# Optimization experiments

Measured on AMD Instinct MI355X. Metric: run time of the kernel, lower is better.

The kernel has to match this reference:

```python
import jax, jax.numpy as jnp
import numpy as np

NEG_SLOPE = 0.2
STRONG_CONVEXITY = 0.5


def _scalar(x, Wq, Wl, bl, Wz, wz_out, wq_out, wl_out):
    # x: [B, D]; Wq/Wl: [L, H, D]; bl: [L, H]; Wz: [L-1, H, H]
    # Precompute all per-layer x-dependent terms in two batched einsums.
    qx = jnp.einsum('lhd,bd->lbh', Wq, x) ** 2          # [L, B, H]
    lx = jnp.einsum('lhd,bd->lbh', Wl, x) + bl[:, None, :]  # [L, B, H]
    z = jax.nn.leaky_relu(qx[0] + lx[0], negative_slope=NEG_SLOPE)

    def step(z, inputs):
        W, q, l = inputs
        z = jax.nn.leaky_relu(z @ W.T + q + l, negative_slope=NEG_SLOPE)
        return z, None

    z, _ = jax.lax.scan(step, z, (Wz, qx[1:], lx[1:]))
    # Final layer to scalar output (no bias on last wx_lin per torch code).
    out = z @ wz_out.T + (x @ wq_out.T) ** 2 + x @ wl_out.T  # [B, 1]
    return out


def setup_inputs() -> dict:
    key = jax.random.key(0)
    ks = jax.random.split(key, 8)
    B, D, H, L = 8192, 128, 512, 10
    f32 = jnp.float32
    x = jax.random.normal(ks[0], (B, D), f32)
    Wq = jax.random.normal(ks[1], (L, H, D), f32) * (1.0 / np.sqrt(D))
    Wl = jax.random.normal(ks[2], (L, H, D), f32) * (1.0 / np.sqrt(D))
    bl = jax.random.normal(ks[3], (L, H), f32) * 0.01
    # wz weights are kept non-negative in the original (clamp/exp init)
    Wz = jnp.abs(jax.random.normal(ks[4], (L - 1, H, H), f32)) * (1.0 / np.sqrt(H))
    wz_out = jnp.abs(jax.random.normal(ks[5], (1, H), f32)) * (1.0 / np.sqrt(H))
    wq_out = jax.random.normal(ks[6], (1, D), f32) * (1.0 / np.sqrt(D))
    wl_out = jax.random.normal(ks[7], (1, D), f32) * (1.0 / np.sqrt(D))
    return {"x": x, "Wq": Wq, "Wl": Wl, "bl": bl, "Wz": Wz,
            "wz_out": wz_out, "wq_out": wq_out, "wl_out": wl_out}


def reference(x, Wq, Wl, bl, Wz, wz_out, wq_out, wl_out):
    # forward = (1 - mu) * d(scalar)/dx + mu * x, with grad_outputs = ones
    def scalar_sum(xx):
        return jnp.sum(_scalar(xx, Wq, Wl, bl, Wz, wz_out, wq_out, wl_out))

    gx = jax.grad(scalar_sum)(x)  # per-sample gradient, [B, D]
    return (1.0 - STRONG_CONVEXITY) * gx + STRONG_CONVEXITY * x
```

## Files before the change

### kernel.cpp

```cpp
#include <hip/hip_runtime.h>


#define Bn 8192
#define Dn 128
#define Hn 512
#define Ln 10
#define NW (Ln * Hn)

constexpr float NS = 0.2f;

typedef __attribute__((ext_vector_type(8))) short short8;
typedef __attribute__((ext_vector_type(4))) float f32x4;

typedef const __attribute__((address_space(1))) void GV;
typedef __attribute__((address_space(3))) void LV;

__device__ __forceinline__ void gload16(const void* g, void* l) {
    __builtin_amdgcn_global_load_lds((GV*)g, (LV*)l, 16, 0, 0);
}

#define MFMA(acc, a, b) acc = __builtin_amdgcn_mfma_f32_16x16x32_bf16(a, b, acc, 0, 0, 0)

__device__ __forceinline__ unsigned short bf16_rne(float v) {
    unsigned u = __float_as_uint(v);
    u += 0x7FFFu + ((u >> 16) & 1u);
    return (unsigned short)(u >> 16);
}
__device__ __forceinline__ float bf2f(unsigned short h) {
    return __uint_as_float(((unsigned)h) << 16);
}
__device__ __forceinline__ void split2(float v, unsigned short& h, unsigned short& l) {
    h = bf16_rne(v);
    l = bf16_rne(v - bf2f(h));
}


__global__ __launch_bounds__(256) void split_flat(const float* __restrict__ in,
        unsigned short* __restrict__ hi, unsigned short* __restrict__ lo, int n4) {
    int i = blockIdx.x * 256 + threadIdx.x;
    if (i >= n4) return;
    float4 v = ((const float4*)in)[i];
    ushort4 h, l;
    split2(v.x, h.x, l.x);
    split2(v.y, h.y, l.y);
    split2(v.z, h.z, l.z);
    split2(v.w, h.w, l.w);
    ((ushort4*)hi)[i] = h;
    ((ushort4*)lo)[i] = l;
}

__global__ __launch_bounds__(256) void transpose_split(const float* __restrict__ in,
        unsigned short* __restrict__ hi, unsigned short* __restrict__ lo, int R, int C) {
    __shared__ float t[32][33];
    const size_t off = (size_t)blockIdx.z * R * C;
    const float* src = in + off;
    unsigned short* dh = hi + off;
    unsigned short* dl = lo + off;
    const int r0 = blockIdx.x * 32, c0 = blockIdx.y * 32;
    const int tr = threadIdx.x >> 5, tc = threadIdx.x & 31;
#pragma unroll
    for (int i = 0; i < 4; ++i)
        t[tr + 8 * i][tc] = src[(size_t)(r0 + tr + 8 * i) * C + c0 + tc];
    __syncthreads();
#pragma unroll
    for (int i = 0; i < 4; ++i) {
        float v = t[tc][tr + 8 * i];
        unsigned short h, l; split2(v, h, l);
        size_t o = (size_t)(c0 + tr + 8 * i) * R + r0 + tc;
        dh[o] = h; dl[o] = l;
    }
}


__global__ __launch_bounds__(256) void gemm_uall(
    const unsigned short* __restrict__ xh, const unsigned short* __restrict__ xl,
    const unsigned short* __restrict__ Wh, const unsigned short* __restrict__ Wv,
    float* __restrict__ u)
{
    __shared__ __align__(16) char smem[32768];
    unsigned short* Ah = (unsigned short*)smem;
    unsigned short* Al = (unsigned short*)(smem + 8192);
    unsigned short* Bh = (unsigned short*)(smem + 16384);
    unsigned short* Bl = (unsigned short*)(smem + 24576);

    const int tid = threadIdx.x;
    const int w = tid >> 6, lane = tid & 63;
    const int lq = lane >> 4, lc = lane & 15;
    const int wm = (w & 1) * 64, wn = (w >> 1) * 64;
    const int row0 = blockIdx.x * 128, col0 = blockIdx.y * 128;
    const int sr = lane >> 2, sk = (lane & 3) * 8;

    f32x4 acc[4][4];
#pragma unroll
    for (int i = 0; i < 4; ++i)
#pragma unroll
        for (int j = 0; j < 4; ++j)
#pragma unroll
            for (int r = 0; r < 4; ++r) acc[i][j][r] = 0.f;

    for (int k0 = 0; k0 < Dn; k0 += 32) {
        __syncthreads();
        for (int c = w; c < 8; c += 4) {
            size_t ga_ = (size_t)(row0 + c * 16 + sr) * Dn + k0 + sk;
            gload16(xh + ga_, Ah + c * 512);
            gload16(xl + ga_, Al + c * 512);
            size_t gb = (size_t)(col0 + c * 16 + sr) * Dn + k0 + sk;
            gload16(Wh + gb, Bh + c * 512);
            gload16(Wv + gb, Bl + c * 512);
        }
        __syncthreads();
        short8 ah[4], al[4];
#pragma unroll
        for (int mt = 0; mt < 4; ++mt) {
            int ao = (wm + mt * 16 + lc) * 32 + lq * 8;
            ah[mt] = *(const short8*)(Ah + ao);
            al[mt] = *(const short8*)(Al + ao);
        }
#pragma unroll
        for (int nt = 0; nt < 4; ++nt) {
            int bo = (wn + nt * 16 + lc) * 32 + lq * 8;
            short8 bh = *(const short8*)(Bh + bo);
            short8 bv = *(const short8*)(Bl + bo);
#pragma unroll
            for (int mt = 0; mt < 4; ++mt) {
                MFMA(acc[mt][nt], ah[mt], bh);
                MFMA(acc[mt][nt], ah[mt], bv);
                MFMA(acc[mt][nt], al[mt], bh);
            }
        }
    }

#pragma unroll
    for (int nt = 0; nt < 4; ++nt) {
        const int col = col0 + wn + nt * 16 + lc;
#pragma unroll
        for (int mt = 0; mt < 4; ++mt) {
            const int rowb = row0 + wm + mt * 16;
#pragma unroll
            for (int r = 0; r < 4; ++r)
                u[(size_t)(rowb + lq * 4 + r) * NW + col] = acc[mt][nt][r];
        }
    }
}


__global__ __launch_bounds__(256) void fwd_mfma(
    const unsigned short* __restrict__ xh, const unsigned short* __restrict__ xl,
    const unsigned short* __restrict__ zph, const unsigned short* __restrict__ zpl,
    const unsigned short* __restrict__ Wzh, const unsigned short* __restrict__ Wzl,
    const unsigned short* __restrict__ Wlh, const unsigned short* __restrict__ Wll,
    const float* __restrict__ bl,
    const float* __restrict__ u,
    unsigned short* __restrict__ zoh, unsigned short* __restrict__ zol,
    unsigned short* __restrict__ mask16, int hasZ)
{
    __shared__ __align__(16) char smem[24576];
    unsigned short* Ah = (unsigned short*)smem;
    unsigned short* Al = (unsigned short*)(smem + 8192);
    unsigned short* Bh = (unsigned short*)(smem + 16384);
    unsigned short* Bl = (unsigned short*)(smem + 20480);

    const int tid = threadIdx.x;
    const int w = tid >> 6, lane = tid & 63;
    const int lq = lane >> 4, lc = lane & 15;
    const int wm = (w & 1) * 64, wn = (w >> 1) * 32;
    const int row0 = blockIdx.x * 128, col0 = blockIdx.y * 64;
    const int sr = lane >> 2, sk = (lane & 3) * 8;

    f32x4 acc[4][2];
#pragma unroll
    for (int i = 0; i < 4; ++i)
#pragma unroll
        for (int j = 0; j < 2; ++j)
#pragma unroll
            for (int r = 0; r < 4; ++r) acc[i][j][r] = 0.f;

    if (hasZ) {
        for (int k0 = 0; k0 < Hn; k0 += 32) {
            __syncthreads();
            for (int c = w; c < 8; c += 4) {
                size_t go = (size_t)(row0 + c * 16 + sr) * Hn + k0 + sk;
                gload16(zph + go, Ah + c * 512);
                gload16(zpl + go, Al + c * 512);
            }
            {
                int c = w;
                size_t go = (size_t)(col0 + c * 16 + sr) * Hn + k0 + sk;
                gload16(Wzh + go, Bh + c * 512);
                gload16(Wzl + go, Bl + c * 512);
            }
            __syncthreads();
            short8 ah[4], al[4];
#pragma unroll
            for (int mt = 0; mt < 4; ++mt) {
                int ao = (wm + mt * 16 + lc) * 32 + lq * 8;
                ah[mt] = *(const short8*)(Ah + ao);
                al[mt] = *(const short8*)(Al + ao);
            }
#pragma unroll
            for (int nt = 0; nt < 2; ++nt) {
                int bo = (wn + nt * 16 + lc) * 32 + lq * 8;
                short8 bh = *(const short8*)(Bh + bo);
                short8 bv = *(const short8*)(Bl + bo);
#pragma unroll
                for (int mt = 0; mt < 4; ++mt) {
                    MFMA(acc[mt][nt], ah[mt], bh);
                    MFMA(acc[mt][nt], ah[mt], bv);
                    MFMA(acc[mt][nt], al[mt], bh);
                }
            }
        }
    }

    for (int k0 = 0; k0 < Dn; k0 += 32) {
        __syncthreads();
        for (int c = w; c < 8; c += 4) {
            size_t go = (size_t)(row0 + c * 16 + sr) * Dn + k0 + sk;
            gload16(xh + go, Ah + c * 512);
            gload16(xl + go, Al + c * 512);
        }
        {
            int c = w;
            size_t go = (size_t)(col0 + c * 16 + sr) * Dn + k0 + sk;
            gload16(Wlh + go, Bh + c * 512);
            gload16(Wll + go, Bl + c * 512);
        }
        __syncthreads();
        short8 ah[4], al[4];
#pragma unroll
        for (int mt = 0; mt < 4; ++mt) {
            int ao = (wm + mt * 16 + lc) * 32 + lq * 8;
            ah[mt] = *(const short8*)(Ah + ao);
            al[mt] = *(const short8*)(Al + ao);
        }
#pragma unroll
        for (int nt = 0; nt < 2; ++nt) {
            int bo = (wn + nt * 16 + lc) * 32 + lq * 8;
            short8 bh = *(const short8*)(Bh + bo);
            short8 bv = *(const short8*)(Bl + bo);
#pragma unroll
            for (int mt = 0; mt < 4; ++mt) {
                MFMA(acc[mt][nt], ah[mt], bh);
                MFMA(acc[mt][nt], ah[mt], bv);
                MFMA(acc[mt][nt], al[mt], bh);
            }
        }
    }

#pragma unroll
    for (int nt = 0; nt < 2; ++nt) {
        const int colb = col0 + wn + nt * 16;
        const int col = colb + lc;
        const float blv = bl[col];
#pragma unroll
        for (int mt = 0; mt < 4; ++mt) {
            const int rowb = row0 + wm + mt * 16;
#pragma unroll
            for (int r = 0; r < 4; ++r) {
                const int row = rowb + lq * 4 + r;
                float uq = u[(size_t)row * NW + col];
                float pre = acc[mt][nt][r] + uq * uq + blv;
                bool m = pre >= 0.f;
                unsigned long long bal = __ballot(m);
                if (lc == 0) {
                    mask16[(size_t)row * 32 + (colb >> 4)] =
                        (unsigned short)((bal >> (lq * 16)) & 0xFFFFull);
                }
                float zv = m ? pre : NS * pre;
                unsigned short h, l; split2(zv, h, l);
                size_t o = (size_t)row * Hn + col;
                zoh[o] = h; zol[o] = l;
            }
        }
    }
}


__global__ __launch_bounds__(256) void bwd_mfma(
    const unsigned short* __restrict__ gah, const unsigned short* __restrict__ gal,
    const unsigned short* __restrict__ WzTh, const unsigned short* __restrict__ WzTl,
    const unsigned short* __restrict__ maskprev,
    unsigned short* __restrict__ goh, unsigned short* __restrict__ gol,
    const float* __restrict__ u,
    const unsigned short* __restrict__ WqTh, const unsigned short* __restrict__ WqTl,
    const unsigned short* __restrict__ WlTh, const unsigned short* __restrict__ WlTl,
    float* __restrict__ gx, int addTo, int nWz)
{
    __shared__ __align__(16) char smem[49152];
    const int tid = threadIdx.x;
    const int w = tid >> 6, lane = tid & 63;
    const int lq = lane >> 4, lc = lane & 15;
    const int wm = (w & 1) * 64, wn = (w >> 1) * 32;
    const int row0 = blockIdx.x * 128;
    const int sr = lane >> 2, sk = (lane & 3) * 8;

    f32x4 acc[4][2];
#pragma unroll
    for (int i = 0; i < 4; ++i)
#pragma unroll
        for (int j = 0; j < 2; ++j)
#pragma unroll
            for (int r = 0; r < 4; ++r) acc[i][j][r] = 0.f;

    if ((int)blockIdx.y < nWz) {
        const int col0 = blockIdx.y * 64;
        unsigned short* Ah = (unsigned short*)smem;
        unsigned short* Al = (unsigned short*)(smem + 8192);
        unsigned short* Bh = (unsigned short*)(smem + 16384);
        unsigned short* Bl = (unsigned short*)(smem + 20480);

        for (int k0 = 0; k0 < Hn; k0 += 32) {
            __syncthreads();
            for (int c = w; c < 8; c += 4) {
                size_t go = (size_t)(row0 + c * 16 + sr) * Hn + k0 + sk;
                gload16(gah + go, Ah + c * 512);
                gload16(gal + go, Al + c * 512);
            }
            {
                int c = w;
                size_t go = (size_t)(col0 + c * 16 + sr) * Hn + k0 + sk;
                gload16(WzTh + go, Bh + c * 512);
                gload16(WzTl + go, Bl + c * 512);
            }
            __syncthreads();
            short8 ah[4], al[4];
#pragma unroll
            for (int mt = 0; mt < 4; ++mt) {
                int ao = (wm + mt * 16 + lc) * 32 + lq * 8;
                ah[mt] = *(const short8*)(Ah + ao);
                al[mt] = *(const short8*)(Al + ao);
            }
#pragma unroll
            for (int nt = 0; nt < 2; ++nt) {
                int bo = (wn + nt * 16 + lc) * 32 + lq * 8;
                short8 bh = *(const short8*)(Bh + bo);
                short8 bv = *(const short8*)(Bl + bo);
#pragma unroll
                for (int mt = 0; mt < 4; ++mt) {
                    MFMA(acc[mt][nt], ah[mt], bh);
                    MFMA(acc[mt][nt], ah[mt], bv);
                    MFMA(acc[mt][nt], al[mt], bh);
                }
            }
        }

#pragma unroll
        for (int nt = 0; nt < 2; ++nt) {
            const int colb = col0 + wn + nt * 16;
            const int col = colb + lc;
#pragma unroll
            for (int mt = 0; mt < 4; ++mt) {
                const int rowb = row0 + wm + mt * 16;
#pragma unroll
                for (int r = 0; r < 4; ++r) {
                    int row = rowb + lq * 4 + r;
                    unsigned short wbits = maskprev[(size_t)row * 32 + (colb >> 4)];
                    float f = ((wbits >> lc) & 1) ? 1.f : NS;
                    float v = acc[mt][nt][r] * f;
                    unsigned short h, l; split2(v, h, l);
                    size_t o = (size_t)row * Hn + col;
                    goh[o] = h; gol[o] = l;
                }
            }
        }
    } else {
        const int col0 = ((int)blockIdx.y - nWz) * 64;
        unsigned short* A1h = (unsigned short*)smem;
        unsigned short* A1l = (unsigned short*)(smem + 8192);
        unsigned short* A2h = (unsigned short*)(smem + 16384);
        unsigned short* A2l = (unsigned short*)(smem + 24576);
        unsigned short* Bqh = (unsigned short*)(smem + 32768);
        unsigned short* Bql = (unsigned short*)(smem + 36864);
        unsigned short* Blh = (unsigned short*)(smem + 40960);
        unsigned short* Bll = (unsigned short*)(smem + 45056);

        const int ar = tid >> 1;
        const int as = (tid & 1) * 16;

        for (int k0 = 0; k0 < Hn; k0 += 32) {
            __syncthreads();
            {
                int c = w;
                size_t go = (size_t)(col0 + c * 16 + sr) * Hn + k0 + sk;
                gload16(WqTh + go, Bqh + c * 512);
                gload16(WqTl + go, Bql + c * 512);
                gload16(WlTh + go, Blh + c * 512);
                gload16(WlTl + go, Bll + c * 512);
            }
            {
                size_t gb = (size_t)(row0 + ar) * Hn + k0 + as;
                const float* urow = u + (size_t)(row0 + ar) * NW + k0 + as;
                int lo_ = ar * 32 + as;
#pragma unroll
                for (int t4 = 0; t4 < 4; ++t4) {
                    float4 uv = *(const float4*)(urow + t4 * 4);
                    ushort4 h = *(const ushort4*)(gah + gb + t4 * 4);
                    ushort4 lw = *(const ushort4*)(gal + gb + t4 * 4);
                    *(ushort4*)(A2h + lo_ + t4 * 4) = h;
                    *(ushort4*)(A2l + lo_ + t4 * 4) = lw;
                    ushort4 oh, ol;
                    float g, a1;
                    g = bf2f(h.x) + bf2f(lw.x); a1 = 2.f * uv.x * g; split2(a1, oh.x, ol.x);
                    g = bf2f(h.y) + bf2f(lw.y); a1 = 2.f * uv.y * g; split2(a1, oh.y, ol.y);
                    g = bf2f(h.z) + bf2f(lw.z); a1 = 2.f * uv.z * g; split2(a1, oh.z, ol.z);
                    g = bf2f(h.w) + bf2f(lw.w); a1 = 2.f * uv.w * g; split2(a1, oh.w, ol.w);
                    *(ushort4*)(A1h + lo_ + t4 * 4) = oh;
                    *(ushort4*)(A1l + lo_ + t4 * 4) = ol;
                }
            }
            __syncthreads();
            short8 a1h[4], a1l[4], a2h[4], a2l[4];
#pragma unroll
            for (int mt = 0; mt < 4; ++mt) {
                int ao = (wm + mt * 16 + lc) * 32 + lq * 8;
                a1h[mt] = *(const short8*)(A1h + ao);
                a1l[mt] = *(const short8*)(A1l + ao);
                a2h[mt] = *(const short8*)(A2h + ao);
                a2l[mt] = *(const short8*)(A2l + ao);
            }
#pragma unroll
            for (int nt = 0; nt < 2; ++nt) {
                int bo = (wn + nt * 16 + lc) * 32 + lq * 8;
                short8 qh = *(const short8*)(Bqh + bo);
                short8 ql_ = *(const short8*)(Bql + bo);
                short8 lh = *(const short8*)(Blh + bo);
                short8 ll_ = *(const short8*)(Bll + bo);
#pragma unroll
                for (int mt = 0; mt < 4; ++mt) {
                    MFMA(acc[mt][nt], a1h[mt], qh);
                    MFMA(acc[mt][nt], a1h[mt], ql_);
                    MFMA(acc[mt][nt], a1l[mt], qh);
                    MFMA(acc[mt][nt], a2h[mt], lh);
                    MFMA(acc[mt][nt], a2h[mt], ll_);
                    MFMA(acc[mt][nt], a2l[mt], lh);
                }
            }
        }

#pragma unroll
        for (int nt = 0; nt < 2; ++nt) {
            const int col = col0 + wn + nt * 16 + lc;
#pragma unroll
            for (int mt = 0; mt < 4; ++mt) {
                const int rowb = row0 + wm + mt * 16;
#pragma unroll
                for (int r = 0; r < 4; ++r) {
                    size_t o = (size_t)(rowb + lq * 4 + r) * Dn + col;
                    float v = acc[mt][nt][r];
                    if (addTo) v += gx[o];
                    gx[o] = v;
                }
            }
        }
    }
}


__global__ __launch_bounds__(256) void ga_init(
    const float* __restrict__ wz_out, const unsigned short* __restrict__ mask9,
    unsigned short* __restrict__ gh, unsigned short* __restrict__ gl)
{
    int i = blockIdx.x * 256 + threadIdx.x;
    int e = i << 2;
    int b = e >> 9, h = e & 511;
    unsigned short wbits = mask9[(size_t)b * 32 + (h >> 4)];
    float4 wv = *(const float4*)(wz_out + h);
    int sh = h & 15;
    ushort4 oh, ol;
    float f;
    f = wv.x * (((wbits >> (sh + 0)) & 1) ? 1.f : NS); split2(f, oh.x, ol.x);
    f = wv.y * (((wbits >> (sh + 1)) & 1) ? 1.f : NS); split2(f, oh.y, ol.y);
    f = wv.z * (((wbits >> (sh + 2)) & 1) ? 1.f : NS); split2(f, oh.z, ol.z);
    f = wv.w * (((wbits >> (sh + 3)) & 1) ? 1.f : NS); split2(f, oh.w, ol.w);
    *(ushort4*)(gh + e) = oh;
    *(ushort4*)(gl + e) = ol;
}

__global__ __launch_bounds__(256) void rowdot_kernel(
    const float* __restrict__ x, const float* __restrict__ wq_out, float* __restrict__ s) {
    const int b = blockIdx.x * 4 + (threadIdx.x >> 6);
    const int lane = threadIdx.x & 63;
    float v = x[(size_t)b * Dn + lane] * wq_out[lane] +
              x[(size_t)b * Dn + 64 + lane] * wq_out[64 + lane];
#pragma unroll
    for (int off = 32; off > 0; off >>= 1) v += __shfl_down(v, off, 64);
    if (lane == 0) s[b] = v;
}

__global__ __launch_bounds__(256) void final_kernel(
    float* __restrict__ out, const float* __restrict__ x, const float* __restrict__ s,
    const float* __restrict__ wq_out, const float* __restrict__ wl_out) {
    const int i = blockIdx.x * 256 + threadIdx.x;
    const int base = i << 2;
    const int b = base >> 7;
    const int d = base & (Dn - 1);
    float4 g = *(const float4*)(out + base);
    float4 xv = *(const float4*)(x + base);
    float4 wq = *(const float4*)(wq_out + d);
    float4 wl = *(const float4*)(wl_out + d);
    const float sb = s[b];
    float4 o;
    o.x = 0.5f * g.x + sb * wq.x + 0.5f * wl.x + 0.5f * xv.x;
    o.y = 0.5f * g.y + sb * wq.y + 0.5f * wl.y + 0.5f * xv.y;
    o.z = 0.5f * g.z + sb * wq.z + 0.5f * wl.z + 0.5f * xv.z;
    o.w = 0.5f * g.w + sb * wq.w + 0.5f * wl.w + 0.5f * xv.w;
    *(float4*)(out + base) = o;
}


extern "C" void kernel_launch(void* const* d_in, const int* in_sizes, int n_in,
                              void* d_out, int out_size, void* d_ws, size_t ws_size,
                              hipStream_t stream) {
    (void)in_sizes; (void)n_in; (void)out_size; (void)ws_size;
    const float* x      = (const float*)d_in[0];
    const float* Wq     = (const float*)d_in[1];
    const float* Wl     = (const float*)d_in[2];
    const float* bl     = (const float*)d_in[3];
    const float* Wz     = (const float*)d_in[4];
    const float* wz_out = (const float*)d_in[5];
    const float* wq_out = (const float*)d_in[6];
    const float* wl_out = (const float*)d_in[7];
    float* out = (float*)d_out;

    char* p = (char*)d_ws;
    #define CARVE(name, bytes) unsigned short* name = (unsigned short*)p; p += (((size_t)(bytes)) + 255) & ~(size_t)255;
    CARVE(xh,  (size_t)Bn*Dn*2)  CARVE(xl,  (size_t)Bn*Dn*2)
    CARVE(Wqh, (size_t)Ln*Hn*Dn*2) CARVE(Wql, (size_t)Ln*Hn*Dn*2)
    CARVE(Wlh, (size_t)Ln*Hn*Dn*2) CARVE(Wll, (size_t)Ln*Hn*Dn*2)
    CARVE(WqTh,(size_t)Ln*Hn*Dn*2) CARVE(WqTl,(size_t)Ln*Hn*Dn*2)
    CARVE(WlTh,(size_t)Ln*Hn*Dn*2) CARVE(WlTl,(size_t)Ln*Hn*Dn*2)
    CARVE(Wzh, (size_t)(Ln-1)*Hn*Hn*2) CARVE(Wzl, (size_t)(Ln-1)*Hn*Hn*2)
    CARVE(WzTh,(size_t)(Ln-1)*Hn*Hn*2) CARVE(WzTl,(size_t)(Ln-1)*Hn*Hn*2)
    CARVE(zAh, (size_t)Bn*Hn*2) CARVE(zAl, (size_t)Bn*Hn*2)
    CARVE(zBh, (size_t)Bn*Hn*2) CARVE(zBl, (size_t)Bn*Hn*2)
    CARVE(mask16, (size_t)Ln*Bn*32*2)
    float* s = (float*)p; p += (size_t)Bn*4 + 256;
    float* uall = (float*)p; p += (size_t)Bn*NW*4;
    #undef CARVE

    split_flat<<<(Bn*Dn/4 + 255)/256, 256, 0, stream>>>(x, xh, xl, Bn*Dn/4);
    split_flat<<<(Ln*Hn*Dn/4 + 255)/256, 256, 0, stream>>>(Wq, Wqh, Wql, Ln*Hn*Dn/4);
    split_flat<<<(Ln*Hn*Dn/4 + 255)/256, 256, 0, stream>>>(Wl, Wlh, Wll, Ln*Hn*Dn/4);
    split_flat<<<((Ln-1)*Hn*Hn/4 + 255)/256, 256, 0, stream>>>(Wz, Wzh, Wzl, (Ln-1)*Hn*Hn/4);
    transpose_split<<<dim3(Hn/32, Dn/32, Ln), 256, 0, stream>>>(Wq, WqTh, WqTl, Hn, Dn);
    transpose_split<<<dim3(Hn/32, Dn/32, Ln), 256, 0, stream>>>(Wl, WlTh, WlTl, Hn, Dn);
    transpose_split<<<dim3(Hn/32, Hn/32, Ln-1), 256, 0, stream>>>(Wz, WzTh, WzTl, Hn, Hn);

    rowdot_kernel<<<Bn/4, 256, 0, stream>>>(x, wq_out, s);

    gemm_uall<<<dim3(Bn/128, NW/128), 256, 0, stream>>>(xh, xl, Wqh, Wql, uall);

    const dim3 gF(Bn/128, Hn/64);

    fwd_mfma<<<gF, 256, 0, stream>>>(xh, xl, nullptr, nullptr, nullptr, nullptr,
        Wlh, Wll, bl, uall, zAh, zAl, mask16, 0);
    for (int l = 1; l < Ln; ++l) {
        const unsigned short* zh  = (l & 1) ? zAh : zBh;
        const unsigned short* zl_ = (l & 1) ? zAl : zBl;
        unsigned short* oh  = (l & 1) ? zBh : zAh;
        unsigned short* ol_ = (l & 1) ? zBl : zAl;
        fwd_mfma<<<gF, 256, 0, stream>>>(xh, xl, zh, zl_,
            Wzh + (size_t)(l-1)*Hn*Hn, Wzl + (size_t)(l-1)*Hn*Hn,
            Wlh + (size_t)l*Hn*Dn, Wll + (size_t)l*Hn*Dn,
            bl + (size_t)l*Hn, uall + (size_t)l*Hn,
            oh, ol_, mask16 + (size_t)l*Bn*32, 1);
    }

    ga_init<<<(Bn*Hn/4)/256, 256, 0, stream>>>(wz_out, mask16 + (size_t)9*Bn*32, zAh, zAl);
    for (int l = Ln - 1; l >= 0; --l) {
        int sidx = (Ln - 1 - l) & 1;
        const unsigned short* gh_ = sidx ? zBh : zAh;
        const unsigned short* gl_ = sidx ? zBl : zAl;
        unsigned short* oh  = sidx ? zAh : zBh;
        unsigned short* ol_ = sidx ? zAl : zBl;
        const int nWz = (l > 0) ? 8 : 0;
        bwd_mfma<<<dim3(Bn/128, nWz + 2), 256, 0, stream>>>(
            gh_, gl_,
            (l > 0) ? WzTh + (size_t)(l-1)*Hn*Hn : WzTh,
            (l > 0) ? WzTl + (size_t)(l-1)*Hn*Hn : WzTl,
            (l > 0) ? mask16 + (size_t)(l-1)*Bn*32 : mask16,
            oh, ol_,
            uall + (size_t)l*Hn,
            WqTh + (size_t)l*Dn*Hn, WqTl + (size_t)l*Dn*Hn,
            WlTh + (size_t)l*Dn*Hn, WlTl + (size_t)l*Dn*Hn,
            out, (l == Ln - 1) ? 0 : 1, nWz);
    }

    final_kernel<<<(Bn*Dn/4)/256, 256, 0, stream>>>(out, x, s, wq_out, wl_out);
}
```

Measured before the change: 1.026 ms.

## Split backward into separate g and x-gradient kernels with split-K atomics

The combined backward kernel is split in two. One kernel computes the hidden gradient through Wz and, in its epilogue, also produces the 2*u*g operand for the quadratic term. The other computes the x-gradient with smaller tiles, split-K over the hidden dimension, and atomicAdd into a pre-zeroed output. This is meant to fix load imbalance: previously the x-gradient blocks ran a full K=512 loop and did extra work per element alongside the Wz blocks. The cost is more kernel launches, an extra a1 buffer written to and read from global memory, and float atomics that make summation order nondeterministic.

```diff
diff --git a/kernel.cpp b/kernel.cpp
--- a/kernel.cpp
+++ b/kernel.cpp
@@ -276,22 +276,25 @@
 }
 
 
-__global__ __launch_bounds__(256) void bwd_mfma(
+__global__ __launch_bounds__(256) void bwd_g_mfma(
     const unsigned short* __restrict__ gah, const unsigned short* __restrict__ gal,
     const unsigned short* __restrict__ WzTh, const unsigned short* __restrict__ WzTl,
     const unsigned short* __restrict__ maskprev,
+    const float* __restrict__ u,
     unsigned short* __restrict__ goh, unsigned short* __restrict__ gol,
-    const float* __restrict__ u,
-    const unsigned short* __restrict__ WqTh, const unsigned short* __restrict__ WqTl,
-    const unsigned short* __restrict__ WlTh, const unsigned short* __restrict__ WlTl,
-    float* __restrict__ gx, int addTo, int nWz)
+    unsigned short* __restrict__ a1h, unsigned short* __restrict__ a1l)
 {
-    __shared__ __align__(16) char smem[49152];
+    __shared__ __align__(16) char smem[24576];
+    unsigned short* Ah = (unsigned short*)smem;
+    unsigned short* Al = (unsigned short*)(smem + 8192);
+    unsigned short* Bh = (unsigned short*)(smem + 16384);
+    unsigned short* Bl = (unsigned short*)(smem + 20480);
+
     const int tid = threadIdx.x;
     const int w = tid >> 6, lane = tid & 63;
     const int lq = lane >> 4, lc = lane & 15;
     const int wm = (w & 1) * 64, wn = (w >> 1) * 32;
-    const int row0 = blockIdx.x * 128;
+    const int row0 = blockIdx.x * 128, col0 = blockIdx.y * 64;
     const int sr = lane >> 2, sk = (lane & 3) * 8;
 
     f32x4 acc[4][2];
@@ -302,178 +305,186 @@
 #pragma unroll
             for (int r = 0; r < 4; ++r) acc[i][j][r] = 0.f;
 
-    if ((int)blockIdx.y < nWz) {
-        const int col0 = blockIdx.y * 64;
-        unsigned short* Ah = (unsigned short*)smem;
-        unsigned short* Al = (unsigned short*)(smem + 8192);
-        unsigned short* Bh = (unsigned short*)(smem + 16384);
-        unsigned short* Bl = (unsigned short*)(smem + 20480);
-
-        for (int k0 = 0; k0 < Hn; k0 += 32) {
-            __syncthreads();
-            for (int c = w; c < 8; c += 4) {
-                size_t go = (size_t)(row0 + c * 16 + sr) * Hn + k0 + sk;
-                gload16(gah + go, Ah + c * 512);
-                gload16(gal + go, Al + c * 512);
-            }
-            {
-                int c = w;
-                size_t go = (size_t)(col0 + c * 16 + sr) * Hn + k0 + sk;
-                gload16(WzTh + go, Bh + c * 512);
-                gload16(WzTl + go, Bl + c * 512);
-            }
-            __syncthreads();
-            short8 ah[4], al[4];
+    for (int k0 = 0; k0 < Hn; k0 += 32) {
+        __syncthreads();
+        for (int c = w; c < 8; c += 4) {
+            size_t go = (size_t)(row0 + c * 16 + sr) * Hn + k0 + sk;
+            gload16(gah + go, Ah + c * 512);
+            gload16(gal + go, Al + c * 512);
+        }
+        {
+            int c = w;
+            size_t go = (size_t)(col0 + c * 16 + sr) * Hn + k0 + sk;
+            gload16(WzTh + go, Bh + c * 512);
+            gload16(WzTl + go, Bl + c * 512);
+        }
+        __syncthreads();
+        short8 ah[4], al[4];
+#pragma unroll
+        for (int mt = 0; mt < 4; ++mt) {
+            int ao = (wm + mt * 16 + lc) * 32 + lq * 8;
+            ah[mt] = *(const short8*)(Ah + ao);
+            al[mt] = *(const short8*)(Al + ao);
+        }
+#pragma unroll
+        for (int nt = 0; nt < 2; ++nt) {
+            int bo = (wn + nt * 16 + lc) * 32 + lq * 8;
+            short8 bh = *(const short8*)(Bh + bo);
+            short8 bv = *(const short8*)(Bl + bo);
 #pragma unroll
             for (int mt = 0; mt < 4; ++mt) {
-                int ao = (wm + mt * 16 + lc) * 32 + lq * 8;
-                ah[mt] = *(const short8*)(Ah + ao);
-                al[mt] = *(const short8*)(Al + ao);
-            }
-#pragma unroll
-            for (int nt = 0; nt < 2; ++nt) {
-                int bo = (wn + nt * 16 + lc) * 32 + lq * 8;
-                short8 bh = *(const short8*)(Bh + bo);
-                short8 bv = *(const short8*)(Bl + bo);
-#pragma unroll
-                for (int mt = 0; mt < 4; ++mt) {
-                    MFMA(acc[mt][nt], ah[mt], bh);
-                    MFMA(acc[mt][nt], ah[mt], bv);
-                    MFMA(acc[mt][nt], al[mt], bh);
-                }
-            }
-        }
-
+                MFMA(acc[mt][nt], ah[mt], bh);
+                MFMA(acc[mt][nt], ah[mt], bv);
+                MFMA(acc[mt][nt], al[mt], bh);
+            }
+        }
+    }
+
+#pragma unroll
+    for (int nt = 0; nt < 2; ++nt) {
+        const int colb = col0 + wn + nt * 16;
+        const int col = colb + lc;
+#pragma unroll
+        for (int mt = 0; mt < 4; ++mt) {
+            const int rowb = row0 + wm + mt * 16;
+#pragma unroll
+            for (int r = 0; r < 4; ++r) {
+                int row = rowb + lq * 4 + r;
+                unsigned short wbits = maskprev[(size_t)row * 32 + (colb >> 4)];
+                float f = ((wbits >> lc) & 1) ? 1.f : NS;
+                float v = acc[mt][nt][r] * f;
+                unsigned short h, l; split2(v, h, l);
+                size_t o = (size_t)row * Hn + col;
+                goh[o] = h; gol[o] = l;
+                float uv = u[(size_t)row * NW + col];
+                float a1 = 2.f * uv * v;
+                split2(a1, h, l);
+                a1h[o] = h; a1l[o] = l;
+            }
+        }
+    }
+}
+
+
+__global__ __launch_bounds__(256) void bwd_x_mfma(
+    const unsigned short* __restrict__ a1h, const unsigned short* __restrict__ a1l,
+    const unsigned short* __restrict__ a2h, const unsigned short* __restrict__ a2l,
+    const unsigned short* __restrict__ WqTh, const unsigned short* __restrict__ WqTl,
+    const unsigned short* __restrict__ WlTh, const unsigned short* __restrict__ WlTl,
+    float* __restrict__ gx)
+{
+    __shared__ __align__(16) char smem[32768];
+    unsigned short* A1h = (unsigned short*)smem;
+    unsigned short* A1l = (unsigned short*)(smem + 4096);
+    unsigned short* A2h = (unsigned short*)(smem + 8192);
+    unsigned short* A2l = (unsigned short*)(smem + 12288);
+    unsigned short* Bqh = (unsigned short*)(smem + 16384);
+    unsigned short* Bql = (unsigned short*)(smem + 20480);
+    unsigned short* Blh = (unsigned short*)(smem + 24576);
+    unsigned short* Bll = (unsigned short*)(smem + 28672);
+
+    const int tid = threadIdx.x;
+    const int w = tid >> 6, lane = tid & 63;
+    const int lq = lane >> 4, lc = lane & 15;
+    const int wm = (w & 1) * 32, wn = (w >> 1) * 32;
+    const int row0 = blockIdx.x * 64, col0 = blockIdx.y * 64;
+    const int kb = blockIdx.z * 128;
+    const int str = tid >> 2, stk = (tid & 3) * 8;
+
+    f32x4 acc[2][2];
+#pragma unroll
+    for (int i = 0; i < 2; ++i)
+#pragma unroll
+        for (int j = 0; j < 2; ++j)
+#pragma unroll
+            for (int r = 0; r < 4; ++r) acc[i][j][r] = 0.f;
+
+    for (int k0 = kb; k0 < kb + 128; k0 += 32) {
+        __syncthreads();
+        {
+            size_t ga_ = (size_t)(row0 + str) * Hn + k0 + stk;
+            size_t gb = (size_t)(col0 + str) * Hn + k0 + stk;
+            int lo_ = str * 32 + stk;
+            gload16(a1h + ga_, A1h + lo_);
+            gload16(a1l + ga_, A1l + lo_);
+            gload16(a2h + ga_, A2h + lo_);
+            gload16(a2l + ga_, A2l + lo_);
+            gload16(WqTh + gb, Bqh + lo_);
+            gload16(WqTl + gb, Bql + lo_);
+            gload16(WlTh + gb, Blh + lo_);
+            gload16(WlTl + gb, Bll + lo_);
+        }
+        __syncthreads();
+        short8 f1h[2], f1l[2], f2h[2], f2l[2];
+#pragma unroll
+        for (int mt = 0; mt < 2; ++mt) {
+            int ao = (wm + mt * 16 + lc) * 32 + lq * 8;
+            f1h[mt] = *(const short8*)(A1h + ao);
+            f1l[mt] = *(const short8*)(A1l + ao);
+            f2h[mt] = *(const short8*)(A2h + ao);
+            f2l[mt] = *(const short8*)(A2l + ao);
+        }
 #pragma unroll
         for (int nt = 0; nt < 2; ++nt) {
-            const int colb = col0 + wn + nt * 16;
-            const int col = colb + lc;
-#pragma unroll
-            for (int mt = 0; mt < 4; ++mt) {
-                const int rowb = row0 + wm + mt * 16;
-#pragma unroll
-                for (int r = 0; r < 4; ++r) {
-                    int row = rowb + lq * 4 + r;
-                    unsigned short wbits = maskprev[(size_t)row * 32 + (colb >> 4)];
-                    float f = ((wbits >> lc) & 1) ? 1.f : NS;
-                    float v = acc[mt][nt][r] * f;
-                    unsigned short h, l; split2(v, h, l);
-                    size_t o = (size_t)row * Hn + col;
-                    goh[o] = h; gol[o] = l;
-                }
-            }
-        }
-    } else {
-        const int col0 = ((int)blockIdx.y - nWz) * 64;
-        unsigned short* A1h = (unsigned short*)smem;
-        unsigned short* A1l = (unsigned short*)(smem + 8192);
-        unsigned short* A2h = (unsigned short*)(smem + 16384);
-        unsigned short* A2l = (unsigned short*)(smem + 24576);
-        unsigned short* Bqh = (unsigned short*)(smem + 32768);
-        unsigned short* Bql = (unsigned short*)(smem + 36864);
-        unsigned short* Blh = (unsigned short*)(smem + 40960);
-        unsigned short* Bll = (unsigned short*)(smem + 45056);
-
-        const int ar = tid >> 1;
-        const int as = (tid & 1) * 16;
-
-        for (int k0 = 0; k0 < Hn; k0 += 32) {
-            __syncthreads();
-            {
-                int c = w;
-                size_t go = (size_t)(col0 + c * 16 + sr) * Hn + k0 + sk;
-                gload16(WqTh + go, Bqh + c * 512);
-                gload16(WqTl + go, Bql + c * 512);
-                gload16(WlTh + go, Blh + c * 512);
-                gload16(WlTl + go, Bll + c * 512);
-            }
-            {
-                size_t gb = (size_t)(row0 + ar) * Hn + k0 + as;
-                const float* urow = u + (size_t)(row0 + ar) * NW + k0 + as;
-                int lo_ = ar * 32 + as;
-#pragma unroll
-                for (int t4 = 0; t4 < 4; ++t4) {
-                    float4 uv = *(const float4*)(urow + t4 * 4);
-                    ushort4 h = *(const ushort4*)(gah + gb + t4 * 4);
-                    ushort4 lw = *(const ushort4*)(gal + gb + t4 * 4);
-                    *(ushort4*)(A2h + lo_ + t4 * 4) = h;
-                    *(ushort4*)(A2l + lo_ + t4 * 4) = lw;
-                    ushort4 oh, ol;
-                    float g, a1;
-                    g = bf2f(h.x) + bf2f(lw.x); a1 = 2.f * uv.x * g; split2(a1, oh.x, ol.x);
-                    g = bf2f(h.y) + bf2f(lw.y); a1 = 2.f * uv.y * g; split2(a1, oh.y, ol.y);
-                    g = bf2f(h.z) + bf2f(lw.z); a1 = 2.f * uv.z * g; split2(a1, oh.z, ol.z);
-                    g = bf2f(h.w) + bf2f(lw.w); a1 = 2.f * uv.w * g; split2(a1, oh.w, ol.w);
-                    *(ushort4*)(A1h + lo_ + t4 * 4) = oh;
-                    *(ushort4*)(A1l + lo_ + t4 * 4) = ol;
-                }
-            }
-            __syncthreads();
-            short8 a1h[4], a1l[4], a2h[4], a2l[4];
-#pragma unroll
-            for (int mt = 0; mt < 4; ++mt) {
-                int ao = (wm + mt * 16 + lc) * 32 + lq * 8;
-                a1h[mt] = *(const short8*)(A1h + ao);
-                a1l[mt] = *(const short8*)(A1l + ao);
-                a2h[mt] = *(const short8*)(A2h + ao);
-                a2l[mt] = *(const short8*)(A2l + ao);
-            }
-#pragma unroll
-            for (int nt = 0; nt < 2; ++nt) {
-                int bo = (wn + nt * 16 + lc) * 32 + lq * 8;
-                short8 qh = *(const short8*)(Bqh + bo);
-                short8 ql_ = *(const short8*)(Bql + bo);
-                short8 lh = *(const short8*)(Blh + bo);
-                short8 ll_ = *(const short8*)(Bll + bo);
-#pragma unroll
-                for (int mt = 0; mt < 4; ++mt) {
-                    MFMA(acc[mt][nt], a1h[mt], qh);
-                    MFMA(acc[mt][nt], a1h[mt], ql_);
-                    MFMA(acc[mt][nt], a1l[mt], qh);
-                    MFMA(acc[mt][nt], a2h[mt], lh);
-                    MFMA(acc[mt][nt], a2h[mt], ll_);
-                    MFMA(acc[mt][nt], a2l[mt], lh);
-                }
-            }
-        }
-
-#pragma unroll
-        for (int nt = 0; nt < 2; ++nt) {
-            const int col = col0 + wn + nt * 16 + lc;
-#pragma unroll
-            for (int mt = 0; mt < 4; ++mt) {
-                const int rowb = row0 + wm + mt * 16;
-#pragma unroll
-                for (int r = 0; r < 4; ++r) {
-                    size_t o = (size_t)(rowb + lq * 4 + r) * Dn + col;
-                    float v = acc[mt][nt][r];
-                    if (addTo) v += gx[o];
-                    gx[o] = v;
-                }
-            }
-        }
-    }
-}
-
+            int bo = (wn + nt * 16 + lc) * 32 + lq * 8;
+            short8 qh = *(const short8*)(Bqh + bo);
+            short8 ql_ = *(const short8*)(Bql + bo);
+            short8 lh = *(const short8*)(Blh + bo);
+            short8 ll_ = *(const short8*)(Bll + bo);
+#pragma unroll
+            for (int mt = 0; mt < 2; ++mt) {
+                MFMA(acc[mt][nt], f1h[mt], qh);
+                MFMA(acc[mt][nt], f1h[mt], ql_);
+                MFMA(acc[mt][nt], f1l[mt], qh);
+                MFMA(acc[mt][nt], f2h[mt], lh);
+                MFMA(acc[mt][nt], f2h[mt], ll_);
+                MFMA(acc[mt][nt], f2l[mt], lh);
+            }
+        }
+    }
+
+#pragma unroll
+    for (int nt = 0; nt < 2; ++nt) {
+        const int col = col0 + wn + nt * 16 + lc;
+#pragma unroll
+        for (int mt = 0; mt < 2; ++mt) {
+            const int rowb = row0 + wm + mt * 16;
+#pragma unroll
+            for (int r = 0; r < 4; ++r)
+                atomicAdd(&gx[(size_t)(rowb + lq * 4 + r) * Dn + col], acc[mt][nt][r]);
+        }
+    }
+}
+
+
+__global__ __launch_bounds__(256) void zero_out(float* __restrict__ p, int n4) {
+    int i = blockIdx.x * 256 + threadIdx.x;
+    if (i < n4) ((float4*)p)[i] = make_float4(0.f, 0.f, 0.f, 0.f);
+}
 
 __global__ __launch_bounds__(256) void ga_init(
     const float* __restrict__ wz_out, const unsigned short* __restrict__ mask9,
-    unsigned short* __restrict__ gh, unsigned short* __restrict__ gl)
+    const float* __restrict__ u9,
+    unsigned short* __restrict__ gh, unsigned short* __restrict__ gl,
+    unsigned short* __restrict__ a1h, unsigned short* __restrict__ a1l)
 {
     int i = blockIdx.x * 256 + threadIdx.x;
     int e = i << 2;
     int b = e >> 9, h = e & 511;
     unsigned short wbits = mask9[(size_t)b * 32 + (h >> 4)];
     float4 wv = *(const float4*)(wz_out + h);
+    float4 uv = *(const float4*)(u9 + (size_t)b * NW + h);
     int sh = h & 15;
-    ushort4 oh, ol;
+    ushort4 oh, ol, th, tl;
     float f;
-    f = wv.x * (((wbits >> (sh + 0)) & 1) ? 1.f : NS); split2(f, oh.x, ol.x);
-    f = wv.y * (((wbits >> (sh + 1)) & 1) ? 1.f : NS); split2(f, oh.y, ol.y);
-    f = wv.z * (((wbits >> (sh + 2)) & 1) ? 1.f : NS); split2(f, oh.z, ol.z);
-    f = wv.w * (((wbits >> (sh + 3)) & 1) ? 1.f : NS); split2(f, oh.w, ol.w);
+    f = wv.x * (((wbits >> (sh + 0)) & 1) ? 1.f : NS); split2(f, oh.x, ol.x); split2(2.f * uv.x * f, th.x, tl.x);
+    f = wv.y * (((wbits >> (sh + 1)) & 1) ? 1.f : NS); split2(f, oh.y, ol.y); split2(2.f * uv.y * f, th.y, tl.y);
+    f = wv.z * (((wbits >> (sh + 2)) & 1) ? 1.f : NS); split2(f, oh.z, ol.z); split2(2.f * uv.z * f, th.z, tl.z);
+    f = wv.w * (((wbits >> (sh + 3)) & 1) ? 1.f : NS); split2(f, oh.w, ol.w); split2(2.f * uv.w * f, th.w, tl.w);
     *(ushort4*)(gh + e) = oh;
     *(ushort4*)(gl + e) = ol;
+    *(ushort4*)(a1h + e) = th;
+    *(ushort4*)(a1l + e) = tl;
 }
 
 __global__ __launch_bounds__(256) void rowdot_kernel(
@@ -533,6 +544,7 @@
     CARVE(WzTh,(size_t)(Ln-1)*Hn*Hn*2) CARVE(WzTl,(size_t)(Ln-1)*Hn*Hn*2)
     CARVE(zAh, (size_t)Bn*Hn*2) CARVE(zAl, (size_t)Bn*Hn*2)
     CARVE(zBh, (size_t)Bn*Hn*2) CARVE(zBl, (size_t)Bn*Hn*2)
+    CARVE(a1h, (size_t)Bn*Hn*2) CARVE(a1l, (size_t)Bn*Hn*2)
     CARVE(mask16, (size_t)Ln*Bn*32*2)
     float* s = (float*)p; p += (size_t)Bn*4 + 256;
     float* uall = (float*)p; p += (size_t)Bn*NW*4;
@@ -566,24 +578,27 @@
             oh, ol_, mask16 + (size_t)l*Bn*32, 1);
     }
 
-    ga_init<<<(Bn*Hn/4)/256, 256, 0, stream>>>(wz_out, mask16 + (size_t)9*Bn*32, zAh, zAl);
+    zero_out<<<(Bn*Dn/4 + 255)/256, 256, 0, stream>>>(out, Bn*Dn/4);
+    ga_init<<<(Bn*Hn/4)/256, 256, 0, stream>>>(wz_out, mask16 + (size_t)9*Bn*32,
+        uall + (size_t)9*Hn, zAh, zAl, a1h, a1l);
+
     for (int l = Ln - 1; l >= 0; --l) {
         int sidx = (Ln - 1 - l) & 1;
         const unsigned short* gh_ = sidx ? zBh : zAh;
         const unsigned short* gl_ = sidx ? zBl : zAl;
-        unsigned short* oh  = sidx ? zAh : zBh;
-        unsigned short* ol_ = sidx ? zAl : zBl;
-        const int nWz = (l > 0) ? 8 : 0;
-        bwd_mfma<<<dim3(Bn/128, nWz + 2), 256, 0, stream>>>(
-            gh_, gl_,
-            (l > 0) ? WzTh + (size_t)(l-1)*Hn*Hn : WzTh,
-            (l > 0) ? WzTl + (size_t)(l-1)*Hn*Hn : WzTl,
-            (l > 0) ? mask16 + (size_t)(l-1)*Bn*32 : mask16,
-            oh, ol_,
-            uall + (size_t)l*Hn,
+        bwd_x_mfma<<<dim3(Bn/64, Dn/64, 4), 256, 0, stream>>>(
+            a1h, a1l, gh_, gl_,
             WqTh + (size_t)l*Dn*Hn, WqTl + (size_t)l*Dn*Hn,
-            WlTh + (size_t)l*Dn*Hn, WlTl + (size_t)l*Dn*Hn,
-            out, (l == Ln - 1) ? 0 : 1, nWz);
+            WlTh + (size_t)l*Dn*Hn, WlTl + (size_t)l*Dn*Hn, out);
+        if (l > 0) {
+            unsigned short* oh  = sidx ? zAh : zBh;
+            unsigned short* ol_ = sidx ? zAl : zBl;
+            bwd_g_mfma<<<gF, 256, 0, stream>>>(gh_, gl_,
+                WzTh + (size_t)(l-1)*Hn*Hn, WzTl + (size_t)(l-1)*Hn*Hn,
+                mask16 + (size_t)(l-1)*Bn*32,
+                uall + (size_t)(l-1)*Hn,
+                oh, ol_, a1h, a1l);
+        }
     }
 
     final_kernel<<<(Bn*Dn/4)/256, 256, 0, stream>>>(out, x, s, wq_out, wl_out);
```

Result: slower. 1.123 ms (+9.4%).
